# Kernel tuning notes

Hardware: AMD Instinct MI355X
Metric: run time of the kernel (lower is better)

## Reference

```python
import jax, jax.numpy as jnp
import numpy as np

TOP_K = 8


def setup_inputs() -> dict:
    key = jax.random.key(0)
    ks = jax.random.split(key, 5)
    B, S, H, E, I = 2, 1024, 2048, 64, 768
    return {
        "hidden_states": jax.random.normal(ks[0], (B, S, H), dtype=jnp.float32),
        "router_w": jax.random.normal(ks[1], (H, E), dtype=jnp.float32) * 0.02,
        "gate_w": jax.random.normal(ks[2], (E, H, I), dtype=jnp.float32) * 0.02,
        "up_w": jax.random.normal(ks[3], (E, H, I), dtype=jnp.float32) * 0.02,
        "down_w": jax.random.normal(ks[4], (E, I, H), dtype=jnp.float32) * 0.02,
    }


def reference(hidden_states, router_w, gate_w, up_w, down_w):
    B, S, H = hidden_states.shape
    E = router_w.shape[1]
    x = hidden_states.reshape(-1, H)                      # [T, H]
    T = x.shape[0]

    router_logits = x @ router_w                           # [T, E]
    probs = jax.nn.softmax(router_logits.astype(jnp.float32), axis=-1)
    topk_w, topk_idx = jax.lax.top_k(probs, TOP_K)         # [T, K]
    topk_w = topk_w / jnp.sum(topk_w, axis=-1, keepdims=True)  # norm_topk_prob
    topk_w = topk_w.astype(x.dtype)

    # Dense combine weights: zero for non-selected experts -> same math as the
    # gather/scatter loop, jit-friendly (no data-dependent shapes).
    combine = jnp.zeros((T, E), dtype=x.dtype)
    combine = combine.at[jnp.arange(T)[:, None], topk_idx].set(topk_w)  # [T, E]

    g = jnp.einsum('th,ehi->tei', x, gate_w)               # [T, E, I]
    u = jnp.einsum('th,ehi->tei', x, up_w)                 # [T, E, I]
    h = jax.nn.silu(g) * u                                 # SwiGLU
    out = jnp.einsum('te,tei,eih->th', combine, h, down_w)  # weighted combine

    return out.reshape(B, S, H), router_logits
```

## Files before the change

### kernel.cpp

```cpp
#include <hip/hip_runtime.h>
#include <hip/hip_bf16.h>

typedef __hip_bfloat16 bf16;
typedef short s16x8 __attribute__((ext_vector_type(8)));
typedef unsigned short u16x8 __attribute__((ext_vector_type(8)));
typedef float f32x4 __attribute__((ext_vector_type(4)));

#define T_TOK 2048
#define HDIM  2048
#define NEXP  64
#define IDIM  768
#define TOPK  8
#define OUT_OFF (T_TOK * HDIM)
#define NPAIR (T_TOK * TOPK)

#define WS_TOPK_IDX  0
#define WS_TOPK_W    (64 * 1024)
#define WS_PAIR_TOK  (128 * 1024)
#define WS_SLOT_OF   (192 * 1024)
#define WS_COUNTS    (256 * 1024)
#define WS_OFFSETS   (257 * 1024)
#define WS_CURSOR    (258 * 1024)
#define WS_H         (1024 * 1024)
#define WS_PARTIAL   (WS_H + (size_t)NPAIR * IDIM * 2)
#define WS_XB        WS_PARTIAL

__device__ __forceinline__ float bf_to_f(unsigned short u) {
    return __uint_as_float(((unsigned int)u) << 16);
}
__device__ __forceinline__ unsigned short f2bf(float f) {
    unsigned int u = __float_as_uint(f);
    unsigned int r = (u + 0x7FFFu + ((u >> 16) & 1u)) >> 16;
    return (unsigned short)r;
}
__device__ __forceinline__ unsigned cvtpk(float lo, float hi) {
    unsigned r;
    asm("v_cvt_pk_bf16_f32 %0, %1, %2" : "=v"(r) : "v"(lo), "v"(hi));
    return r;
}

typedef const __attribute__((address_space(1))) unsigned int* gas_ptr;
typedef __attribute__((address_space(3))) unsigned int* las_ptr;
__device__ __forceinline__ void gload_lds16(const void* g, void* l) {
    __builtin_amdgcn_global_load_lds((gas_ptr)g, (las_ptr)l, 16, 0, 0);
}

__global__ __launch_bounds__(256) void xbf_kernel(const float* __restrict__ x,
                                                  unsigned short* __restrict__ xb) {
    int i = blockIdx.x * 256 + threadIdx.x;
    const float4* src = (const float4*)x + (size_t)i * 2;
    float4 a = src[0], b = src[1];
    u16x8 o;
    o[0] = f2bf(a.x); o[1] = f2bf(a.y); o[2] = f2bf(a.z); o[3] = f2bf(a.w);
    o[4] = f2bf(b.x); o[5] = f2bf(b.y); o[6] = f2bf(b.z); o[7] = f2bf(b.w);
    ((u16x8*)xb)[i] = o;
}

__global__ __launch_bounds__(256) void router_kernel(
    const float* __restrict__ x, const float* __restrict__ rw,
    float* __restrict__ logits) {
    int wave = threadIdx.x >> 6;
    int lane = threadIdx.x & 63;
    int t = blockIdx.x * 4 + wave;
    const float4* x4 = (const float4*)(x + (size_t)t * HDIM);
    float acc = 0.f;
    for (int h4 = 0; h4 < HDIM / 4; ++h4) {
        float4 xv = x4[h4];
        int h = h4 * 4;
        acc = fmaf(xv.x, rw[(h + 0) * NEXP + lane], acc);
        acc = fmaf(xv.y, rw[(h + 1) * NEXP + lane], acc);
        acc = fmaf(xv.z, rw[(h + 2) * NEXP + lane], acc);
        acc = fmaf(xv.w, rw[(h + 3) * NEXP + lane], acc);
    }
    logits[t * NEXP + lane] = acc;
}

__global__ __launch_bounds__(64) void topk_kernel(
    const float* __restrict__ logits, int* __restrict__ topk_idx,
    float* __restrict__ topk_w, int* __restrict__ counts) {
    int t = blockIdx.x;
    int lane = threadIdx.x;
    float lg = logits[t * NEXP + lane];
    float mx = lg;
    for (int off = 32; off; off >>= 1) mx = fmaxf(mx, __shfl_xor(mx, off));
    float ex = expf(lg - mx);
    float sum = ex;
    for (int off = 32; off; off >>= 1) sum += __shfl_xor(sum, off);
    float prob = ex / sum;

    float pr = prob;
    float myv = 0.f;
    int myidx = 0;
    float ksum = 0.f;
    for (int k = 0; k < TOPK; ++k) {
        float v = pr;
        int idx = lane;
        for (int off = 32; off; off >>= 1) {
            float ov = __shfl_xor(v, off);
            int oi = __shfl_xor(idx, off);
            if (ov > v || (ov == v && oi < idx)) { v = ov; idx = oi; }
        }
        ksum += v;
        if (lane == k) { myidx = idx; myv = v; }
        if (lane == idx) pr = -1.f;
    }
    if (lane < TOPK) {
        topk_idx[t * TOPK + lane] = myidx;
        topk_w[t * TOPK + lane] = myv / ksum;
        atomicAdd(&counts[myidx], 1);
    }
}

__global__ __launch_bounds__(64) void scan_kernel(
    const int* __restrict__ counts, int* __restrict__ offsets, int* __restrict__ cursor) {
    int lane = threadIdx.x;
    int c = counts[lane];
    int incl = c;
    for (int off = 1; off < 64; off <<= 1) {
        int tt = __shfl_up(incl, off);
        if (lane >= off) incl += tt;
    }
    offsets[lane] = incl - c;
    if (lane == 63) offsets[64] = incl;
    cursor[lane] = 0;
}

__global__ __launch_bounds__(256) void scatter_kernel(
    const int* __restrict__ topk_idx, const int* __restrict__ offsets,
    int* __restrict__ cursor, int* __restrict__ pair_token, int* __restrict__ slot_of) {
    int i = blockIdx.x * 256 + threadIdx.x;
    if (i >= NPAIR) return;
    int t = i >> 3;
    int e = topk_idx[i];
    int pos = atomicAdd(&cursor[e], 1);
    int slot = offsets[e] + pos;
    pair_token[slot] = t;
    slot_of[i] = slot;
}

#define BM   256
#define BKS  64
#define NZG  6
#define NZD  8
#define NKG  (HDIM / BKS)
#define NKD  (IDIM / BKS)

__global__ __launch_bounds__(1024, 4) void gateup_mfma(
    const unsigned short* __restrict__ xb, const float* __restrict__ gate_w,
    const float* __restrict__ up_w, const int* __restrict__ offsets,
    const int* __restrict__ pair_token, unsigned short* __restrict__ hbuf) {
    int id = blockIdx.x;
    int b = id & 7, g = id >> 3;
    int ntile = g % NZG;
    int e = b + 8 * (g / NZG);
    int off = offsets[e];
    int cnt = offsets[e + 1] - off;
    if (cnt <= 0) return;

    __shared__ unsigned short As[2][BM * BKS];
    __shared__ unsigned short Bgu[2][256 * BKS];
    __shared__ int toks[BM];

    int tid = threadIdx.x;
    int lane = tid & 63;
    int w = tid >> 6;
    int wr = w & 3, wc = w >> 2;
    int l15 = lane & 15, lg4 = lane >> 4;

    int mat = tid >> 9;
    int s = tid & 511;
    int nI2 = s & 63, kC = s >> 6;
    int brow0 = mat * 128 + nI2 * 2;
    int bslot = (kC ^ (nI2 & 7)) * 8;
    const float* bsrc = (mat ? up_w : gate_w) + (size_t)e * HDIM * IDIM
                        + (size_t)(kC * 8) * IDIM + ntile * 128 + nI2 * 2;

    int arow = tid >> 3;
    int ajx = (tid & 7) ^ (arow & 7);

    for (int mt = 0; mt * BM < cnt; ++mt) {
        int m0 = mt * BM;
        if (tid < BM) {
            int p = m0 + tid;
            toks[tid] = pair_token[off + (p < cnt ? p : 0)];
        }
        __syncthreads();
        const unsigned short* aq[2];
        aq[0] = xb + (size_t)toks[arow] * HDIM + ajx * 8;
        aq[1] = xb + (size_t)toks[arow + 128] * HDIM + ajx * 8;
        f32x4 accg[4][2] = {};
        f32x4 accu[4][2] = {};

        gload_lds16(aq[0], &As[0][tid * 8]);
        gload_lds16(aq[1], &As[0][(1024 + tid) * 8]);
        float2 Bv[8];
        #pragma unroll
        for (int i = 0; i < 8; ++i)
            Bv[i] = *(const float2*)(bsrc + (size_t)i * IDIM);

        for (int ks = 0; ks < NKG; ++ks) {
            int p = ks & 1;
            {
                uint4 w0, w1;
                w0.x = cvtpk(Bv[0].x, Bv[1].x); w0.y = cvtpk(Bv[2].x, Bv[3].x);
                w0.z = cvtpk(Bv[4].x, Bv[5].x); w0.w = cvtpk(Bv[6].x, Bv[7].x);
                w1.x = cvtpk(Bv[0].y, Bv[1].y); w1.y = cvtpk(Bv[2].y, Bv[3].y);
                w1.z = cvtpk(Bv[4].y, Bv[5].y); w1.w = cvtpk(Bv[6].y, Bv[7].y);
                *(uint4*)&Bgu[p][brow0 * BKS + bslot] = w0;
                *(uint4*)&Bgu[p][(brow0 + 1) * BKS + bslot] = w1;
            }
            __syncthreads();
            if (ks + 1 < NKG) {
                int h1 = (ks + 1) * BKS;
                gload_lds16(aq[0] + h1, &As[p ^ 1][tid * 8]);
                gload_lds16(aq[1] + h1, &As[p ^ 1][(1024 + tid) * 8]);
                #pragma unroll
                for (int i = 0; i < 8; ++i)
                    Bv[i] = *(const float2*)(bsrc + (size_t)(h1 + i) * IDIM);
            }
            #pragma unroll
            for (int kk = 0; kk < 2; ++kk) {
                int jk = kk * 4 + lg4;
                s16x8 a[4], bg[2], bu[2];
                #pragma unroll
                for (int mr = 0; mr < 4; ++mr) {
                    int r = wr * 64 + mr * 16 + l15;
                    a[mr] = *(const s16x8*)&As[p][r * BKS + ((jk ^ (r & 7)) * 8)];
                }
                #pragma unroll
                for (int nr = 0; nr < 2; ++nr) {
                    int rg = wc * 32 + nr * 16 + l15;
                    int ru = 128 + rg;
                    bg[nr] = *(const s16x8*)&Bgu[p][rg * BKS + ((jk ^ ((rg >> 1) & 7)) * 8)];
                    bu[nr] = *(const s16x8*)&Bgu[p][ru * BKS + ((jk ^ ((ru >> 1) & 7)) * 8)];
                }
                #pragma unroll
                for (int mr = 0; mr < 4; ++mr)
                    #pragma unroll
                    for (int nr = 0; nr < 2; ++nr) {
                        accg[mr][nr] = __builtin_amdgcn_mfma_f32_16x16x32_bf16(a[mr], bg[nr], accg[mr][nr], 0, 0, 0);
                        accu[mr][nr] = __builtin_amdgcn_mfma_f32_16x16x32_bf16(a[mr], bu[nr], accu[mr][nr], 0, 0, 0);
                    }
            }
        }

        #pragma unroll
        for (int mr = 0; mr < 4; ++mr)
            #pragma unroll
            for (int nr = 0; nr < 2; ++nr) {
                int col = ntile * 128 + wc * 32 + nr * 16 + l15;
                #pragma unroll
                for (int reg = 0; reg < 4; ++reg) {
                    int r = m0 + wr * 64 + mr * 16 + lg4 * 4 + reg;
                    if (r < cnt) {
                        float gv = accg[mr][nr][reg];
                        float uv = accu[mr][nr][reg];
                        float hv = (gv / (1.f + __expf(-gv))) * uv;
                        hbuf[(size_t)(off + r) * IDIM + col] = f2bf(hv);
                    }
                }
            }
        __syncthreads();
    }
}

__global__ __launch_bounds__(1024, 4) void down_mfma(
    const unsigned short* __restrict__ hbuf, const float* __restrict__ down_w,
    const int* __restrict__ offsets, unsigned short* __restrict__ partial) {
    int id = blockIdx.x;
    int b = id & 7, g = id >> 3;
    int ntile = g % NZD;
    int e = b + 8 * (g / NZD);
    int off = offsets[e];
    int cnt = offsets[e + 1] - off;
    if (cnt <= 0) return;

    __shared__ unsigned short As[2][BM * BKS];
    __shared__ unsigned short Bd[2][256 * BKS];

    int tid = threadIdx.x;
    int lane = tid & 63;
    int w = tid >> 6;
    int wr = w & 3, wc = w >> 2;
    int l15 = lane & 15, lg4 = lane >> 4;

    int nI2 = tid & 127, kC = tid >> 7;
    int brow0 = nI2 * 2;
    int bslot = (kC ^ (nI2 & 7)) * 8;
    const float* bsrc = down_w + (size_t)e * IDIM * HDIM
                        + (size_t)(kC * 8) * HDIM + ntile * 256 + nI2 * 2;

    int arow = tid >> 3;
    int ajx = (tid & 7) ^ (arow & 7);

    for (int mt = 0; mt * BM < cnt; ++mt) {
        int m0 = mt * BM;
        __syncthreads();
        int r0 = m0 + arow;       if (r0 >= cnt) r0 = cnt - 1;
        int r1 = m0 + arow + 128; if (r1 >= cnt) r1 = cnt - 1;
        const unsigned short* aq[2];
        aq[0] = hbuf + (size_t)(off + r0) * IDIM + ajx * 8;
        aq[1] = hbuf + (size_t)(off + r1) * IDIM + ajx * 8;
        f32x4 acc[4][4] = {};

        gload_lds16(aq[0], &As[0][tid * 8]);
        gload_lds16(aq[1], &As[0][(1024 + tid) * 8]);
        float2 Bv[8];
        #pragma unroll
        for (int i = 0; i < 8; ++i)
            Bv[i] = *(const float2*)(bsrc + (size_t)i * HDIM);

        for (int ks = 0; ks < NKD; ++ks) {
            int p = ks & 1;
            {
                uint4 w0, w1;
                w0.x = cvtpk(Bv[0].x, Bv[1].x); w0.y = cvtpk(Bv[2].x, Bv[3].x);
                w0.z = cvtpk(Bv[4].x, Bv[5].x); w0.w = cvtpk(Bv[6].x, Bv[7].x);
                w1.x = cvtpk(Bv[0].y, Bv[1].y); w1.y = cvtpk(Bv[2].y, Bv[3].y);
                w1.z = cvtpk(Bv[4].y, Bv[5].y); w1.w = cvtpk(Bv[6].y, Bv[7].y);
                *(uint4*)&Bd[p][brow0 * BKS + bslot] = w0;
                *(uint4*)&Bd[p][(brow0 + 1) * BKS + bslot] = w1;
            }
            __syncthreads();
            if (ks + 1 < NKD) {
                int k1 = (ks + 1) * BKS;
                gload_lds16(aq[0] + k1, &As[p ^ 1][tid * 8]);
                gload_lds16(aq[1] + k1, &As[p ^ 1][(1024 + tid) * 8]);
                #pragma unroll
                for (int i = 0; i < 8; ++i)
                    Bv[i] = *(const float2*)(bsrc + (size_t)(k1 + i) * HDIM);
            }
            #pragma unroll
            for (int kk = 0; kk < 2; ++kk) {
                int jk = kk * 4 + lg4;
                s16x8 a[4], bb[4];
                #pragma unroll
                for (int mr = 0; mr < 4; ++mr) {
                    int r = wr * 64 + mr * 16 + l15;
                    a[mr] = *(const s16x8*)&As[p][r * BKS + ((jk ^ (r & 7)) * 8)];
                }
                #pragma unroll
                for (int nr = 0; nr < 4; ++nr) {
                    int row = wc * 64 + nr * 16 + l15;
                    bb[nr] = *(const s16x8*)&Bd[p][row * BKS + ((jk ^ ((row >> 1) & 7)) * 8)];
                }
                #pragma unroll
                for (int mr = 0; mr < 4; ++mr)
                    #pragma unroll
                    for (int nr = 0; nr < 4; ++nr)
                        acc[mr][nr] = __builtin_amdgcn_mfma_f32_16x16x32_bf16(
                            a[mr], bb[nr], acc[mr][nr], 0, 0, 0);
            }
        }

        #pragma unroll
        for (int mr = 0; mr < 4; ++mr)
            #pragma unroll
            for (int nr = 0; nr < 4; ++nr) {
                int col = ntile * 256 + wc * 64 + nr * 16 + l15;
                #pragma unroll
                for (int reg = 0; reg < 4; ++reg) {
                    int r = m0 + wr * 64 + mr * 16 + lg4 * 4 + reg;
                    if (r < cnt)
                        partial[(size_t)(off + r) * HDIM + col] = f2bf(acc[mr][nr][reg]);
                }
            }
        __syncthreads();
    }
}

__global__ __launch_bounds__(256) void reduce_kernel(
    const unsigned short* __restrict__ partial, const int* __restrict__ slot_of,
    const float* __restrict__ topk_w, float* __restrict__ out) {
    int t = blockIdx.x;
    int j8 = threadIdx.x * 8;
    __shared__ int ss[8];
    __shared__ float sw[8];
    if (threadIdx.x < 8) {
        ss[threadIdx.x] = slot_of[t * TOPK + threadIdx.x];
        sw[threadIdx.x] = topk_w[t * TOPK + threadIdx.x];
    }
    __syncthreads();
    float acc[8] = {};
    #pragma unroll
    for (int k = 0; k < TOPK; ++k) {
        u16x8 v = *(const u16x8*)&partial[(size_t)ss[k] * HDIM + j8];
        float w = sw[k];
        #pragma unroll
        for (int i = 0; i < 8; ++i)
            acc[i] = fmaf(w, bf_to_f((unsigned short)v[i]), acc[i]);
    }
    float4 o0 = {acc[0], acc[1], acc[2], acc[3]};
    float4 o1 = {acc[4], acc[5], acc[6], acc[7]};
    *(float4*)&out[(size_t)t * HDIM + j8] = o0;
    *(float4*)&out[(size_t)t * HDIM + j8 + 4] = o1;
}

extern "C" void kernel_launch(void* const* d_in, const int* in_sizes, int n_in,
                              void* d_out, int out_size, void* d_ws, size_t ws_size,
                              hipStream_t stream) {
    const float* x  = (const float*)d_in[0];
    const float* rw = (const float*)d_in[1];
    const float* gw = (const float*)d_in[2];
    const float* uw = (const float*)d_in[3];
    const float* dw = (const float*)d_in[4];
    float* out = (float*)d_out;
    float* logits = out + OUT_OFF;

    char* ws = (char*)d_ws;
    int*   topk_idx   = (int*)(ws + WS_TOPK_IDX);
    float* topk_w     = (float*)(ws + WS_TOPK_W);
    int*   pair_token = (int*)(ws + WS_PAIR_TOK);
    int*   slot_of    = (int*)(ws + WS_SLOT_OF);
    int*   counts     = (int*)(ws + WS_COUNTS);
    int*   offsets    = (int*)(ws + WS_OFFSETS);
    int*   cursor     = (int*)(ws + WS_CURSOR);
    unsigned short* hbuf    = (unsigned short*)(ws + WS_H);
    unsigned short* partial = (unsigned short*)(ws + WS_PARTIAL);
    unsigned short* xb      = (unsigned short*)(ws + WS_XB);

    hipMemsetAsync(counts, 0, NEXP * sizeof(int), stream);
    xbf_kernel<<<T_TOK * HDIM / (256 * 8), 256, 0, stream>>>(x, xb);
    router_kernel<<<T_TOK / 4, 256, 0, stream>>>(x, rw, logits);
    topk_kernel<<<T_TOK, 64, 0, stream>>>(logits, topk_idx, topk_w, counts);
    scan_kernel<<<1, 64, 0, stream>>>(counts, offsets, cursor);
    scatter_kernel<<<NPAIR / 256, 256, 0, stream>>>(topk_idx, offsets, cursor, pair_token, slot_of);
    gateup_mfma<<<NEXP * NZG, 1024, 0, stream>>>(xb, gw, uw, offsets, pair_token, hbuf);
    down_mfma<<<NEXP * NZD, 1024, 0, stream>>>(hbuf, dw, offsets, partial);
    reduce_kernel<<<dim3(T_TOK, 1), 256, 0, stream>>>(partial, slot_of, topk_w, out);
}
```

Baseline: 734.0 us.

## Halve GEMM block tiles and K-step to 512 threads with padded B layout

Both expert GEMM kernels move from 1024-thread blocks with a 256x256 (gate/up 256x128x2) tile and BKS=64 to 512-thread blocks with half-width N tiles and BKS=32. This doubles the grid (12 and 16 N-tiles per expert) to fill more CUs and raise occupancy. The B tile in LDS now uses padded rows (stride 40) and a new XOR swizzle, and each B fragment is read as two 8-byte loads. In exchange, each block reuses A less and every A row is fetched twice as often across N tiles. The K loop also takes twice as many iterations, so more barriers are paid per unit of work.

```diff
diff --git a/kernel.cpp b/kernel.cpp
--- a/kernel.cpp
+++ b/kernel.cpp
@@ -139,108 +139,108 @@
 }
 
 #define BM   256
-#define BKS  64
-#define NZG  6
-#define NZD  8
+#define BKS  32
+#define BROW 40
 #define NKG  (HDIM / BKS)
 #define NKD  (IDIM / BKS)
 
-__global__ __launch_bounds__(1024, 4) void gateup_mfma(
+__global__ __launch_bounds__(512, 4) void gateup_mfma(
     const unsigned short* __restrict__ xb, const float* __restrict__ gate_w,
     const float* __restrict__ up_w, const int* __restrict__ offsets,
     const int* __restrict__ pair_token, unsigned short* __restrict__ hbuf) {
     int id = blockIdx.x;
-    int b = id & 7, g = id >> 3;
-    int ntile = g % NZG;
-    int e = b + 8 * (g / NZG);
+    int b = id & 7, rid = id >> 3;
+    int ntile = rid % 12;
+    int e = b + 8 * (rid / 12);
     int off = offsets[e];
     int cnt = offsets[e + 1] - off;
     if (cnt <= 0) return;
 
     __shared__ unsigned short As[2][BM * BKS];
-    __shared__ unsigned short Bgu[2][256 * BKS];
+    __shared__ unsigned short Bgu[2][128 * BROW];
     __shared__ int toks[BM];
 
     int tid = threadIdx.x;
     int lane = tid & 63;
-    int w = tid >> 6;
-    int wr = w & 3, wc = w >> 2;
+    int wave = tid >> 6;
+    int wr = wave >> 1, wc = wave & 1;
     int l15 = lane & 15, lg4 = lane >> 4;
 
-    int mat = tid >> 9;
-    int s = tid & 511;
-    int nI2 = s & 63, kC = s >> 6;
-    int brow0 = mat * 128 + nI2 * 2;
-    int bslot = (kC ^ (nI2 & 7)) * 8;
+    int mat = tid >> 8;
+    int rem = tid & 255;
+    int nI2 = rem & 31, kc8 = rem >> 5;
+    int brow = mat * 64 + nI2 * 2;
+    int bslot = (kc8 ^ (nI2 & 7)) * 4;
     const float* bsrc = (mat ? up_w : gate_w) + (size_t)e * HDIM * IDIM
-                        + (size_t)(kC * 8) * IDIM + ntile * 128 + nI2 * 2;
-
-    int arow = tid >> 3;
-    int ajx = (tid & 7) ^ (arow & 7);
+                        + (size_t)(kc8 * 4) * IDIM + ntile * 64 + nI2 * 2;
+
+    int arowq = tid >> 2;
+    int ac = tid & 3;
 
     for (int mt = 0; mt * BM < cnt; ++mt) {
         int m0 = mt * BM;
         if (tid < BM) {
             int p = m0 + tid;
-            toks[tid] = pair_token[off + (p < cnt ? p : 0)];
+            toks[tid] = pair_token[off + (p < cnt ? p : cnt - 1)];
         }
         __syncthreads();
         const unsigned short* aq[2];
-        aq[0] = xb + (size_t)toks[arow] * HDIM + ajx * 8;
-        aq[1] = xb + (size_t)toks[arow + 128] * HDIM + ajx * 8;
+        #pragma unroll
+        for (int q = 0; q < 2; ++q) {
+            int row = q * 128 + arowq;
+            int j2 = ac ^ (row & 3) ^ ((row >> 2) & 3);
+            aq[q] = xb + (size_t)toks[row] * HDIM + j2 * 8;
+        }
         f32x4 accg[4][2] = {};
         f32x4 accu[4][2] = {};
 
         gload_lds16(aq[0], &As[0][tid * 8]);
-        gload_lds16(aq[1], &As[0][(1024 + tid) * 8]);
-        float2 Bv[8];
-        #pragma unroll
-        for (int i = 0; i < 8; ++i)
+        gload_lds16(aq[1], &As[0][(512 + tid) * 8]);
+        float2 Bv[4];
+        #pragma unroll
+        for (int i = 0; i < 4; ++i)
             Bv[i] = *(const float2*)(bsrc + (size_t)i * IDIM);
 
         for (int ks = 0; ks < NKG; ++ks) {
             int p = ks & 1;
             {
-                uint4 w0, w1;
+                uint2 w0, w1;
                 w0.x = cvtpk(Bv[0].x, Bv[1].x); w0.y = cvtpk(Bv[2].x, Bv[3].x);
-                w0.z = cvtpk(Bv[4].x, Bv[5].x); w0.w = cvtpk(Bv[6].x, Bv[7].x);
                 w1.x = cvtpk(Bv[0].y, Bv[1].y); w1.y = cvtpk(Bv[2].y, Bv[3].y);
-                w1.z = cvtpk(Bv[4].y, Bv[5].y); w1.w = cvtpk(Bv[6].y, Bv[7].y);
-                *(uint4*)&Bgu[p][brow0 * BKS + bslot] = w0;
-                *(uint4*)&Bgu[p][(brow0 + 1) * BKS + bslot] = w1;
+                *(uint2*)&Bgu[p][brow * BROW + bslot] = w0;
+                *(uint2*)&Bgu[p][(brow + 1) * BROW + bslot] = w1;
             }
             __syncthreads();
             if (ks + 1 < NKG) {
                 int h1 = (ks + 1) * BKS;
                 gload_lds16(aq[0] + h1, &As[p ^ 1][tid * 8]);
-                gload_lds16(aq[1] + h1, &As[p ^ 1][(1024 + tid) * 8]);
-                #pragma unroll
-                for (int i = 0; i < 8; ++i)
-                    Bv[i] = *(const float2*)(bsrc + (size_t)(h1 + i) * IDIM);
-            }
-            #pragma unroll
-            for (int kk = 0; kk < 2; ++kk) {
-                int jk = kk * 4 + lg4;
-                s16x8 a[4], bg[2], bu[2];
+                gload_lds16(aq[1] + h1, &As[p ^ 1][(512 + tid) * 8]);
+                #pragma unroll
+                for (int i = 0; i < 4; ++i)
+                    Bv[i] = *(const float2*)(bsrc + (size_t)((ks + 1) * BKS + i) * IDIM);
+            }
+            s16x8 a[4];
+            #pragma unroll
+            for (int mr = 0; mr < 4; ++mr) {
+                int r = wr * 64 + mr * 16 + l15;
+                int sa = lg4 ^ (r & 3) ^ ((r >> 2) & 3);
+                a[mr] = *(const s16x8*)&As[p][r * BKS + sa * 8];
+            }
+            #pragma unroll
+            for (int nr = 0; nr < 2; ++nr) {
+                int ng = wc * 32 + nr * 16 + l15;
+                int s0 = ((2 * lg4) ^ ((ng >> 1) & 7)) * 4;
+                int s1 = ((2 * lg4 + 1) ^ ((ng >> 1) & 7)) * 4;
+                s16x8 bg, bu;
+                *(uint2*)&bg = *(const uint2*)&Bgu[p][ng * BROW + s0];
+                *((uint2*)&bg + 1) = *(const uint2*)&Bgu[p][ng * BROW + s1];
+                *(uint2*)&bu = *(const uint2*)&Bgu[p][(64 + ng) * BROW + s0];
+                *((uint2*)&bu + 1) = *(const uint2*)&Bgu[p][(64 + ng) * BROW + s1];
                 #pragma unroll
                 for (int mr = 0; mr < 4; ++mr) {
-                    int r = wr * 64 + mr * 16 + l15;
-                    a[mr] = *(const s16x8*)&As[p][r * BKS + ((jk ^ (r & 7)) * 8)];
+                    accg[mr][nr] = __builtin_amdgcn_mfma_f32_16x16x32_bf16(a[mr], bg, accg[mr][nr], 0, 0, 0);
+                    accu[mr][nr] = __builtin_amdgcn_mfma_f32_16x16x32_bf16(a[mr], bu, accu[mr][nr], 0, 0, 0);
                 }
-                #pragma unroll
-                for (int nr = 0; nr < 2; ++nr) {
-                    int rg = wc * 32 + nr * 16 + l15;
-                    int ru = 128 + rg;
-                    bg[nr] = *(const s16x8*)&Bgu[p][rg * BKS + ((jk ^ ((rg >> 1) & 7)) * 8)];
-                    bu[nr] = *(const s16x8*)&Bgu[p][ru * BKS + ((jk ^ ((ru >> 1) & 7)) * 8)];
-                }
-                #pragma unroll
-                for (int mr = 0; mr < 4; ++mr)
-                    #pragma unroll
-                    for (int nr = 0; nr < 2; ++nr) {
-                        accg[mr][nr] = __builtin_amdgcn_mfma_f32_16x16x32_bf16(a[mr], bg[nr], accg[mr][nr], 0, 0, 0);
-                        accu[mr][nr] = __builtin_amdgcn_mfma_f32_16x16x32_bf16(a[mr], bu[nr], accu[mr][nr], 0, 0, 0);
-                    }
             }
         }
 
@@ -248,14 +248,14 @@
         for (int mr = 0; mr < 4; ++mr)
             #pragma unroll
             for (int nr = 0; nr < 2; ++nr) {
-                int col = ntile * 128 + wc * 32 + nr * 16 + l15;
+                int col = ntile * 64 + wc * 32 + nr * 16 + l15;
                 #pragma unroll
                 for (int reg = 0; reg < 4; ++reg) {
                     int r = m0 + wr * 64 + mr * 16 + lg4 * 4 + reg;
                     if (r < cnt) {
-                        float gv = accg[mr][nr][reg];
-                        float uv = accu[mr][nr][reg];
-                        float hv = (gv / (1.f + __expf(-gv))) * uv;
+                        float g = accg[mr][nr][reg];
+                        float u = accu[mr][nr][reg];
+                        float hv = (g / (1.f + __expf(-g))) * u;
                         hbuf[(size_t)(off + r) * IDIM + col] = f2bf(hv);
                     }
                 }
@@ -264,92 +264,92 @@
     }
 }
 
-__global__ __launch_bounds__(1024, 4) void down_mfma(
+__global__ __launch_bounds__(512, 4) void down_mfma(
     const unsigned short* __restrict__ hbuf, const float* __restrict__ down_w,
     const int* __restrict__ offsets, unsigned short* __restrict__ partial) {
     int id = blockIdx.x;
-    int b = id & 7, g = id >> 3;
-    int ntile = g % NZD;
-    int e = b + 8 * (g / NZD);
+    int b = id & 7, rid = id >> 3;
+    int ntile = rid % 16;
+    int e = b + 8 * (rid / 16);
     int off = offsets[e];
     int cnt = offsets[e + 1] - off;
     if (cnt <= 0) return;
 
     __shared__ unsigned short As[2][BM * BKS];
-    __shared__ unsigned short Bd[2][256 * BKS];
+    __shared__ unsigned short Bd[2][128 * BROW];
 
     int tid = threadIdx.x;
     int lane = tid & 63;
-    int w = tid >> 6;
-    int wr = w & 3, wc = w >> 2;
+    int wave = tid >> 6;
+    int wr = wave >> 1, wc = wave & 1;
     int l15 = lane & 15, lg4 = lane >> 4;
 
-    int nI2 = tid & 127, kC = tid >> 7;
-    int brow0 = nI2 * 2;
-    int bslot = (kC ^ (nI2 & 7)) * 8;
+    int nI2 = tid & 63, kc8 = tid >> 6;
+    int brow = nI2 * 2;
+    int bslot = (kc8 ^ (nI2 & 7)) * 4;
     const float* bsrc = down_w + (size_t)e * IDIM * HDIM
-                        + (size_t)(kC * 8) * HDIM + ntile * 256 + nI2 * 2;
-
-    int arow = tid >> 3;
-    int ajx = (tid & 7) ^ (arow & 7);
+                        + (size_t)(kc8 * 4) * HDIM + ntile * 128 + nI2 * 2;
+
+    int arowq = tid >> 2;
+    int ac = tid & 3;
 
     for (int mt = 0; mt * BM < cnt; ++mt) {
         int m0 = mt * BM;
         __syncthreads();
-        int r0 = m0 + arow;       if (r0 >= cnt) r0 = cnt - 1;
-        int r1 = m0 + arow + 128; if (r1 >= cnt) r1 = cnt - 1;
         const unsigned short* aq[2];
-        aq[0] = hbuf + (size_t)(off + r0) * IDIM + ajx * 8;
-        aq[1] = hbuf + (size_t)(off + r1) * IDIM + ajx * 8;
+        #pragma unroll
+        for (int q = 0; q < 2; ++q) {
+            int row = q * 128 + arowq;
+            int rr = m0 + row;
+            if (rr >= cnt) rr = cnt - 1;
+            int j2 = ac ^ (row & 3) ^ ((row >> 2) & 3);
+            aq[q] = hbuf + (size_t)(off + rr) * IDIM + j2 * 8;
+        }
         f32x4 acc[4][4] = {};
 
         gload_lds16(aq[0], &As[0][tid * 8]);
-        gload_lds16(aq[1], &As[0][(1024 + tid) * 8]);
-        float2 Bv[8];
-        #pragma unroll
-        for (int i = 0; i < 8; ++i)
+        gload_lds16(aq[1], &As[0][(512 + tid) * 8]);
+        float2 Bv[4];
+        #pragma unroll
+        for (int i = 0; i < 4; ++i)
             Bv[i] = *(const float2*)(bsrc + (size_t)i * HDIM);
 
         for (int ks = 0; ks < NKD; ++ks) {
             int p = ks & 1;
             {
-                uint4 w0, w1;
+                uint2 w0, w1;
                 w0.x = cvtpk(Bv[0].x, Bv[1].x); w0.y = cvtpk(Bv[2].x, Bv[3].x);
-                w0.z = cvtpk(Bv[4].x, Bv[5].x); w0.w = cvtpk(Bv[6].x, Bv[7].x);
                 w1.x = cvtpk(Bv[0].y, Bv[1].y); w1.y = cvtpk(Bv[2].y, Bv[3].y);
-                w1.z = cvtpk(Bv[4].y, Bv[5].y); w1.w = cvtpk(Bv[6].y, Bv[7].y);
-                *(uint4*)&Bd[p][brow0 * BKS + bslot] = w0;
-                *(uint4*)&Bd[p][(brow0 + 1) * BKS + bslot] = w1;
+                *(uint2*)&Bd[p][brow * BROW + bslot] = w0;
+                *(uint2*)&Bd[p][(brow + 1) * BROW + bslot] = w1;
             }
             __syncthreads();
             if (ks + 1 < NKD) {
                 int k1 = (ks + 1) * BKS;
                 gload_lds16(aq[0] + k1, &As[p ^ 1][tid * 8]);
-                gload_lds16(aq[1] + k1, &As[p ^ 1][(1024 + tid) * 8]);
-                #pragma unroll
-                for (int i = 0; i < 8; ++i)
+                gload_lds16(aq[1] + k1, &As[p ^ 1][(512 + tid) * 8]);
+                #pragma unroll
+                for (int i = 0; i < 4; ++i)
                     Bv[i] = *(const float2*)(bsrc + (size_t)(k1 + i) * HDIM);
             }
-            #pragma unroll
-            for (int kk = 0; kk < 2; ++kk) {
-                int jk = kk * 4 + lg4;
-                s16x8 a[4], bb[4];
-                #pragma unroll
-                for (int mr = 0; mr < 4; ++mr) {
-                    int r = wr * 64 + mr * 16 + l15;
-                    a[mr] = *(const s16x8*)&As[p][r * BKS + ((jk ^ (r & 7)) * 8)];
-                }
-                #pragma unroll
-                for (int nr = 0; nr < 4; ++nr) {
-                    int row = wc * 64 + nr * 16 + l15;
-                    bb[nr] = *(const s16x8*)&Bd[p][row * BKS + ((jk ^ ((row >> 1) & 7)) * 8)];
-                }
+            s16x8 a[4];
+            #pragma unroll
+            for (int mr = 0; mr < 4; ++mr) {
+                int r = wr * 64 + mr * 16 + l15;
+                int sa = lg4 ^ (r & 3) ^ ((r >> 2) & 3);
+                a[mr] = *(const s16x8*)&As[p][r * BKS + sa * 8];
+            }
+            #pragma unroll
+            for (int nr = 0; nr < 4; ++nr) {
+                int n = wc * 64 + nr * 16 + l15;
+                int s0 = ((2 * lg4) ^ ((n >> 1) & 7)) * 4;
+                int s1 = ((2 * lg4 + 1) ^ ((n >> 1) & 7)) * 4;
+                s16x8 bb;
+                *(uint2*)&bb = *(const uint2*)&Bd[p][n * BROW + s0];
+                *((uint2*)&bb + 1) = *(const uint2*)&Bd[p][n * BROW + s1];
                 #pragma unroll
                 for (int mr = 0; mr < 4; ++mr)
-                    #pragma unroll
-                    for (int nr = 0; nr < 4; ++nr)
-                        acc[mr][nr] = __builtin_amdgcn_mfma_f32_16x16x32_bf16(
-                            a[mr], bb[nr], acc[mr][nr], 0, 0, 0);
+                    acc[mr][nr] = __builtin_amdgcn_mfma_f32_16x16x32_bf16(a[mr], bb, acc[mr][nr], 0, 0, 0);
             }
         }
 
@@ -357,7 +357,7 @@
         for (int mr = 0; mr < 4; ++mr)
             #pragma unroll
             for (int nr = 0; nr < 4; ++nr) {
-                int col = ntile * 256 + wc * 64 + nr * 16 + l15;
+                int col = ntile * 128 + wc * 64 + nr * 16 + l15;
                 #pragma unroll
                 for (int reg = 0; reg < 4; ++reg) {
                     int r = m0 + wr * 64 + mr * 16 + lg4 * 4 + reg;
@@ -425,7 +425,7 @@
     topk_kernel<<<T_TOK, 64, 0, stream>>>(logits, topk_idx, topk_w, counts);
     scan_kernel<<<1, 64, 0, stream>>>(counts, offsets, cursor);
     scatter_kernel<<<NPAIR / 256, 256, 0, stream>>>(topk_idx, offsets, cursor, pair_token, slot_of);
-    gateup_mfma<<<NEXP * NZG, 1024, 0, stream>>>(xb, gw, uw, offsets, pair_token, hbuf);
-    down_mfma<<<NEXP * NZD, 1024, 0, stream>>>(hbuf, dw, offsets, partial);
+    gateup_mfma<<<NEXP * 12, 512, 0, stream>>>(xb, gw, uw, offsets, pair_token, hbuf);
+    down_mfma<<<NEXP * 16, 512, 0, stream>>>(hbuf, dw, offsets, partial);
     reduce_kernel<<<dim3(T_TOK, 1), 256, 0, stream>>>(partial, slot_of, topk_w, out);
 }
```

Result: faster. 714.2 us (-2.7%).
